# Optimization experiments

Hardware: AMD Instinct MI355X
Metric: run time of the kernel (lower is better)

The kernel has to match this reference:

```python
import jax, jax.numpy as jnp
import numpy as np


def _conv_s2(x, w):
    # NCHW input, OIHW weights, stride 2, VALID padding
    return jax.lax.conv_general_dilated(
        x, w, window_strides=(2, 2), padding='VALID',
        dimension_numbers=('NCHW', 'OIHW', 'NCHW'))


def setup_inputs() -> dict:
    key = jax.random.key(0)
    ks = jax.random.split(key, 9)
    B = 65536
    winit = lambda k, fan_in, shape: (jax.random.uniform(k, shape) - 0.5) * 2 * 2.4 / fan_in ** 0.5
    return {
        'x': jax.random.normal(ks[0], (B, 1, 16, 16), dtype=jnp.float32),
        'H1w': winit(ks[1], 5 * 5 * 1, (12, 1, 5, 5)),
        'H1b': jnp.zeros((12, 8, 8), dtype=jnp.float32),
        'H2w': winit(ks[2], 5 * 5 * 8, (12, 8, 5, 5)),
        'H2b': jnp.zeros((12, 4, 4), dtype=jnp.float32),
        'H3w': winit(ks[3], 4 * 4 * 12, (4 * 4 * 12, 30)),
        'H3b': jnp.zeros((30,), dtype=jnp.float32),
        'outw': winit(ks[4], 30, (30, 10)),
        'outb': -jnp.ones((10,), dtype=jnp.float32),
    }


def reference(x, H1w, H1b, H2w, H2b, H3w, H3b, outw, outb):
    NEG1_PAD = ((0, 0), (0, 0), (2, 2), (2, 2))
    # H1: pad 16->20 with -1, 5x5 conv stride 2 -> [B,12,8,8]
    x = jnp.pad(x, NEG1_PAD, constant_values=-1.0)
    x = jnp.tanh(_conv_s2(x, H1w) + H1b)
    # H2: pad 8->12 with -1, three group convs over 8-of-12 channels -> [B,12,4,4]
    x = jnp.pad(x, NEG1_PAD, constant_values=-1.0)
    s1 = _conv_s2(x[:, 0:8], H2w[0:4])
    s2 = _conv_s2(x[:, 4:12], H2w[4:8])
    s3 = _conv_s2(jnp.concatenate((x[:, 0:4], x[:, 8:12]), axis=1), H2w[8:12])
    x = jnp.tanh(jnp.concatenate((s1, s2, s3), axis=1) + H2b)
    # H3 + output MLP
    x = x.reshape(x.shape[0], -1)  # [B,192]
    x = jnp.tanh(x @ H3w + H3b)
    x = jnp.tanh(x @ outw + outb)
    return x
```

## Files before the change

### kernel.cpp

```cpp
#include <hip/hip_runtime.h>

typedef __attribute__((ext_vector_type(8))) short short8;
typedef __attribute__((ext_vector_type(4))) float f32x4;

#define SPB 4
#define NG  8
#define XP_S   400
#define A1_ROW 14
#define A1_CH  (12 * A1_ROW)
#define A1_S   (12 * A1_CH)
#define A2_S   200
#define A3_S   40

__device__ __forceinline__ float fast_tanh(float x) {
    float e = __builtin_amdgcn_exp2f(x * 2.8853900817779268f);
    return 1.0f - 2.0f * __builtin_amdgcn_rcpf(e + 1.0f);
}
__device__ __forceinline__ unsigned short f2bf(float f) {
    unsigned u = __builtin_bit_cast(unsigned, f);
    return (unsigned short)((u + 0x7FFF + ((u >> 16) & 1)) >> 16);
}


__global__ __launch_bounds__(256, 3) void lenet_mfma(
    const float* __restrict__ x,
    const float* __restrict__ w1, const float* __restrict__ b1,
    const float* __restrict__ w2, const float* __restrict__ b2,
    const float* __restrict__ w3, const float* __restrict__ b3,
    const float* __restrict__ ow, const float* __restrict__ ob,
    float* __restrict__ out)
{
    __shared__ __attribute__((aligned(16))) unsigned short wf3[6144];
    __shared__ __attribute__((aligned(16))) unsigned short xp[SPB * XP_S];
    __shared__ __attribute__((aligned(16))) unsigned short a1[SPB * A1_S];
    __shared__ __attribute__((aligned(16))) unsigned short a2[16 * A2_S];
    __shared__ __attribute__((aligned(16))) unsigned short a3[16 * A3_S];
    __shared__ float b1s[768], b2s[192], b3s[32], obs[16];

    const int t = threadIdx.x;
    const int lane = t & 63, wv = t >> 6;
    const int hi = lane >> 4, col = lane & 15;

    const float4* xg = (const float4*)(x + (size_t)blockIdx.x * NG * SPB * 256);
    float4 v0 = xg[t];

    int po1[4], po2[4];
    #pragma unroll
    for (int pp = 0; pp < 4; ++pp) {
        int P = 4 * hi + pp; if (P > 14) P = 14;
        int ky = P / 3, q = P - 3 * ky;
        po1[pp] = ky * 20 + 2 * q;
        po2[pp] = ky * A1_ROW + 2 * q;
    }

    short8 aw1;
    #pragma unroll
    for (int j = 0; j < 8; ++j) {
        int m = 8 * hi + j; float val = 0.f;
        if (m < 30 && col < 12) {
            int P = m >> 1, ky = P / 3, q = P - 3 * ky, c = 2 * q + (m & 1);
            if (c < 5) val = w1[col * 25 + ky * 5 + c];
        }
        aw1[j] = (short)f2bf(val);
    }
    short8 aw2[12];
    #pragma unroll
    for (int ic = 0; ic < 12; ++ic) {
        #pragma unroll
        for (int j = 0; j < 8; ++j) {
            int m = 8 * hi + j; float val = 0.f;
            if (m < 30 && col < 12) {
                int P = m >> 1, ky = P / 3, q = P - 3 * ky, c = 2 * q + (m & 1);
                if (c < 5) {
                    int oc = col, icw;
                    if (oc < 4)      icw = (ic < 8) ? ic : -1;
                    else if (oc < 8) icw = (ic >= 4) ? ic - 4 : -1;
                    else             icw = (ic < 4) ? ic : ((ic >= 8) ? ic - 4 : -1);
                    if (icw >= 0) val = w2[(oc * 8 + icw) * 25 + ky * 5 + c];
                }
            }
            aw2[ic][j] = (short)f2bf(val);
        }
    }
    short8 awo;
    #pragma unroll
    for (int j = 0; j < 8; ++j) {
        int k = 8 * hi + j;
        awo[j] = (short)f2bf((col < 10 && k < 30) ? ow[k * 10 + col] : 0.f);
    }

    for (int e = t; e < 768; e += 256) {
        int fi = e >> 6, le = e & 63;
        int rt = fi / 6, kt = fi - 6 * rt;
        int unit = rt * 16 + (le & 15);
        short8 v;
        #pragma unroll
        for (int j = 0; j < 8; ++j) {
            int k = kt * 32 + 8 * (le >> 4) + j;
            v[j] = (short)f2bf((unit < 30) ? w3[k * 30 + unit] : 0.f);
        }
        *((short8*)wf3 + e) = v;
    }

    {
        unsigned* xpw = (unsigned*)xp;
        for (int i = t; i < SPB * XP_S / 2; i += 256) xpw[i] = 0xBF80BF80u;
        unsigned* a1w = (unsigned*)a1;
        for (int i = t; i < SPB * A1_S / 2; i += 256) a1w[i] = 0xBF80BF80u;
        unsigned* a3w = (unsigned*)a3;
        for (int i = t; i < 16 * A3_S / 2; i += 256) a3w[i] = 0u;
        for (int i = t; i < 768; i += 256) b1s[i] = b1[i];
        if (t < 192) b2s[t] = b2[t];
        if (t < 32)  b3s[t] = (t < 30) ? b3[t] : 0.f;
        if (t < 16)  obs[t] = (t < 10) ? ob[t] : 0.f;
    }
    __syncthreads();

    const int q1 = 40 * (col >> 3) + 2 * (col & 7);
    const int q2 = 28 * (col >> 2) + 2 * (col & 3);
    const unsigned* xp32 = (const unsigned*)xp;
    const unsigned* a132 = (const unsigned*)a1;

    #pragma unroll 1
    for (int g = 0; g < NG; ++g) {
        {
            int r = (t >> 2) & 15, c4 = (t & 3) * 4;
            int base = wv * XP_S + (2 + r) * 20 + (2 + c4);
            unsigned* dst = (unsigned*)xp + (base >> 1);
            dst[0] = (unsigned)f2bf(v0.x) | ((unsigned)f2bf(v0.y) << 16);
            dst[1] = (unsigned)f2bf(v0.z) | ((unsigned)f2bf(v0.w) << 16);
        }
        if (g + 1 < NG) v0 = xg[(g + 1) * 256 + t];

        {
            int sbase = wv * XP_S + q1;
            #pragma unroll
            for (int pt = 0; pt < 4; ++pt) {
                int base = (sbase + pt * 80) >> 1;
                short8 b;
                #pragma unroll
                for (int pp = 0; pp < 4; ++pp) {
                    unsigned r = xp32[base + (po1[pp] >> 1)];
                    b[2 * pp]     = (short)(r & 0xffff);
                    b[2 * pp + 1] = (short)(r >> 16);
                }
                f32x4 acc = __builtin_amdgcn_mfma_f32_16x16x32_bf16(
                    aw1, b, (f32x4){0.f, 0.f, 0.f, 0.f}, 0, 0, 0);
                int p = pt * 16 + col;
                int oy = p >> 3, ox = p & 7;
                int wbase = wv * A1_S + (2 + oy) * A1_ROW + (2 + ox);
                #pragma unroll
                for (int jj = 0; jj < 4; ++jj) {
                    int oc = hi * 4 + jj;
                    if (oc < 12)
                        a1[wbase + oc * A1_CH] =
                            f2bf(fast_tanh(acc[jj] + b1s[oc * 64 + p]));
                }
            }
        }

        {
            int sbase = wv * A1_S + q2;
            f32x4 acc = {0.f, 0.f, 0.f, 0.f};
            #pragma unroll
            for (int ic = 0; ic < 12; ++ic) {
                int base = (sbase + ic * A1_CH) >> 1;
                short8 b;
                #pragma unroll
                for (int pp = 0; pp < 4; ++pp) {
                    unsigned r = a132[base + (po2[pp] >> 1)];
                    b[2 * pp]     = (short)(r & 0xffff);
                    b[2 * pp + 1] = (short)(r >> 16);
                }
                acc = __builtin_amdgcn_mfma_f32_16x16x32_bf16(aw2[ic], b, acc, 0, 0, 0);
            }
            int sg = (g & 3) * 4 + wv;
            #pragma unroll
            for (int jj = 0; jj < 4; ++jj) {
                int oc = hi * 4 + jj;
                if (oc < 12)
                    a2[sg * A2_S + oc * 16 + col] =
                        f2bf(fast_tanh(acc[jj] + b2s[oc * 16 + col]));
            }
        }

        if ((g & 3) == 3) {
            __syncthreads();
            if (wv < 2) {
                int rt = wv;
                f32x4 acc = {0.f, 0.f, 0.f, 0.f};
                #pragma unroll
                for (int kt = 0; kt < 6; ++kt) {
                    short8 a = *((const short8*)wf3 + (rt * 6 + kt) * 64 + lane);
                    short8 b = *(const short8*)&a2[col * A2_S + kt * 32 + 8 * hi];
                    acc = __builtin_amdgcn_mfma_f32_16x16x32_bf16(a, b, acc, 0, 0, 0);
                }
                #pragma unroll
                for (int jj = 0; jj < 4; ++jj) {
                    int unit = rt * 16 + hi * 4 + jj;
                    if (unit < 30)
                        a3[col * A3_S + unit] = f2bf(fast_tanh(acc[jj] + b3s[unit]));
                }
            }
            __syncthreads();
            if (wv == 0) {
                short8 b = *(const short8*)&a3[col * A3_S + 8 * hi];
                f32x4 acc = __builtin_amdgcn_mfma_f32_16x16x32_bf16(
                    awo, b, (f32x4){0.f, 0.f, 0.f, 0.f}, 0, 0, 0);
                size_t sw = (size_t)blockIdx.x * (NG * SPB) + (g >> 2) * 16 + col;
                #pragma unroll
                for (int jj = 0; jj < 4; ++jj) {
                    int row = hi * 4 + jj;
                    if (row < 10)
                        out[sw * 10 + row] = fast_tanh(acc[jj] + obs[row]);
                }
            }
            __syncthreads();
        }
    }
}

extern "C" void kernel_launch(void* const* d_in, const int* in_sizes, int n_in,
                              void* d_out, int out_size, void* d_ws, size_t ws_size,
                              hipStream_t stream) {
    const float* x  = (const float*)d_in[0];
    const float* w1 = (const float*)d_in[1];
    const float* b1 = (const float*)d_in[2];
    const float* w2 = (const float*)d_in[3];
    const float* b2 = (const float*)d_in[4];
    const float* w3 = (const float*)d_in[5];
    const float* b3 = (const float*)d_in[6];
    const float* ow = (const float*)d_in[7];
    const float* ob = (const float*)d_in[8];
    float* out = (float*)d_out;

    const int B = in_sizes[0] / 256;
    lenet_mfma<<<dim3(B / (SPB * NG)), dim3(256), 0, stream>>>(
        x, w1, b1, w2, b2, w3, b3, ow, ob, out);
}
```

Before: 111.7 us.

## Shrink LDS footprint, split H2 accumulation chains, and spread FC layers across all waves

Reduces the A1 row pitch from 14 to 12 and stores the H1 bias as bf16 to cut shared memory, and raises launch bounds from 3 to 4 blocks per CU. The H2 convolution now uses two independent MFMA accumulator chains to shorten dependency latency. The H3 and output layers run on all four waves, each handling its own four samples instead of waves 0-1 and wave 0 doing all sixteen. This trades some duplicated MFMA work (only 4 of 16 columns are useful) and bf16 bias rounding for less serialization and higher occupancy.

```diff
diff --git a/kernel.cpp b/kernel.cpp
--- a/kernel.cpp
+++ b/kernel.cpp
@@ -6,7 +6,7 @@
 #define SPB 4
 #define NG  8
 #define XP_S   400
-#define A1_ROW 14
+#define A1_ROW 12
 #define A1_CH  (12 * A1_ROW)
 #define A1_S   (12 * A1_CH)
 #define A2_S   200
@@ -20,9 +20,12 @@
     unsigned u = __builtin_bit_cast(unsigned, f);
     return (unsigned short)((u + 0x7FFF + ((u >> 16) & 1)) >> 16);
 }
-
-
-__global__ __launch_bounds__(256, 3) void lenet_mfma(
+__device__ __forceinline__ float bf2f(unsigned short h) {
+    return __builtin_bit_cast(float, (unsigned)h << 16);
+}
+
+
+__global__ __launch_bounds__(256, 4) void lenet_mfma(
     const float* __restrict__ x,
     const float* __restrict__ w1, const float* __restrict__ b1,
     const float* __restrict__ w2, const float* __restrict__ b2,
@@ -35,7 +38,8 @@
     __shared__ __attribute__((aligned(16))) unsigned short a1[SPB * A1_S];
     __shared__ __attribute__((aligned(16))) unsigned short a2[16 * A2_S];
     __shared__ __attribute__((aligned(16))) unsigned short a3[16 * A3_S];
-    __shared__ float b1s[768], b2s[192], b3s[32], obs[16];
+    __shared__ unsigned short b1s[768];
+    __shared__ float b2s[192], b3s[32], obs[16];
 
     const int t = threadIdx.x;
     const int lane = t & 63, wv = t >> 6;
@@ -109,7 +113,7 @@
         for (int i = t; i < SPB * A1_S / 2; i += 256) a1w[i] = 0xBF80BF80u;
         unsigned* a3w = (unsigned*)a3;
         for (int i = t; i < 16 * A3_S / 2; i += 256) a3w[i] = 0u;
-        for (int i = t; i < 768; i += 256) b1s[i] = b1[i];
+        for (int i = t; i < 768; i += 256) b1s[i] = f2bf(b1[i]);
         if (t < 192) b2s[t] = b2[t];
         if (t < 32)  b3s[t] = (t < 30) ? b3[t] : 0.f;
         if (t < 16)  obs[t] = (t < 10) ? ob[t] : 0.f;
@@ -117,14 +121,15 @@
     __syncthreads();
 
     const int q1 = 40 * (col >> 3) + 2 * (col & 7);
-    const int q2 = 28 * (col >> 2) + 2 * (col & 3);
+    const int q2 = 24 * (col >> 2) + 2 * (col & 3);
     const unsigned* xp32 = (const unsigned*)xp;
     const unsigned* a132 = (const unsigned*)a1;
+    const int colc = col & 3;
 
     #pragma unroll 1
     for (int g = 0; g < NG; ++g) {
         {
-            int r = (t >> 2) & 15, c4 = (t & 3) * 4;
+            int r = lane >> 2, c4 = (lane & 3) * 4;
             int base = wv * XP_S + (2 + r) * 20 + (2 + c4);
             unsigned* dst = (unsigned*)xp + (base >> 1);
             dst[0] = (unsigned)f2bf(v0.x) | ((unsigned)f2bf(v0.y) << 16);
@@ -154,64 +159,71 @@
                     int oc = hi * 4 + jj;
                     if (oc < 12)
                         a1[wbase + oc * A1_CH] =
-                            f2bf(fast_tanh(acc[jj] + b1s[oc * 64 + p]));
+                            f2bf(fast_tanh(acc[jj] + bf2f(b1s[oc * 64 + p])));
                 }
             }
         }
 
         {
             int sbase = wv * A1_S + q2;
-            f32x4 acc = {0.f, 0.f, 0.f, 0.f};
-            #pragma unroll
-            for (int ic = 0; ic < 12; ++ic) {
-                int base = (sbase + ic * A1_CH) >> 1;
-                short8 b;
+            f32x4 acc0 = {0.f, 0.f, 0.f, 0.f};
+            f32x4 acc1 = {0.f, 0.f, 0.f, 0.f};
+            #pragma unroll
+            for (int ic = 0; ic < 6; ++ic) {
+                int b0 = (sbase + ic * A1_CH) >> 1;
+                int b1i = (sbase + (ic + 6) * A1_CH) >> 1;
+                short8 p0, p1;
                 #pragma unroll
                 for (int pp = 0; pp < 4; ++pp) {
-                    unsigned r = a132[base + (po2[pp] >> 1)];
-                    b[2 * pp]     = (short)(r & 0xffff);
-                    b[2 * pp + 1] = (short)(r >> 16);
-                }
-                acc = __builtin_amdgcn_mfma_f32_16x16x32_bf16(aw2[ic], b, acc, 0, 0, 0);
-            }
-            int sg = (g & 3) * 4 + wv;
+                    unsigned r0 = a132[b0 + (po2[pp] >> 1)];
+                    unsigned r1 = a132[b1i + (po2[pp] >> 1)];
+                    p0[2 * pp]     = (short)(r0 & 0xffff);
+                    p0[2 * pp + 1] = (short)(r0 >> 16);
+                    p1[2 * pp]     = (short)(r1 & 0xffff);
+                    p1[2 * pp + 1] = (short)(r1 >> 16);
+                }
+                acc0 = __builtin_amdgcn_mfma_f32_16x16x32_bf16(aw2[ic], p0, acc0, 0, 0, 0);
+                acc1 = __builtin_amdgcn_mfma_f32_16x16x32_bf16(aw2[ic + 6], p1, acc1, 0, 0, 0);
+            }
+            int sg = wv * 4 + (g & 3);
             #pragma unroll
             for (int jj = 0; jj < 4; ++jj) {
                 int oc = hi * 4 + jj;
                 if (oc < 12)
                     a2[sg * A2_S + oc * 16 + col] =
-                        f2bf(fast_tanh(acc[jj] + b2s[oc * 16 + col]));
+                        f2bf(fast_tanh(acc0[jj] + acc1[jj] + b2s[oc * 16 + col]));
             }
         }
 
         if ((g & 3) == 3) {
             __syncthreads();
-            if (wv < 2) {
-                int rt = wv;
+            #pragma unroll
+            for (int rt = 0; rt < 2; ++rt) {
                 f32x4 acc = {0.f, 0.f, 0.f, 0.f};
                 #pragma unroll
                 for (int kt = 0; kt < 6; ++kt) {
                     short8 a = *((const short8*)wf3 + (rt * 6 + kt) * 64 + lane);
-                    short8 b = *(const short8*)&a2[col * A2_S + kt * 32 + 8 * hi];
+                    short8 b = *(const short8*)&a2[(wv * 4 + colc) * A2_S + kt * 32 + 8 * hi];
                     acc = __builtin_amdgcn_mfma_f32_16x16x32_bf16(a, b, acc, 0, 0, 0);
                 }
                 #pragma unroll
                 for (int jj = 0; jj < 4; ++jj) {
                     int unit = rt * 16 + hi * 4 + jj;
-                    if (unit < 30)
-                        a3[col * A3_S + unit] = f2bf(fast_tanh(acc[jj] + b3s[unit]));
+                    if (unit < 30 && col < 4)
+                        a3[(wv * 4 + col) * A3_S + unit] =
+                            f2bf(fast_tanh(acc[jj] + b3s[unit]));
                 }
             }
             __syncthreads();
-            if (wv == 0) {
-                short8 b = *(const short8*)&a3[col * A3_S + 8 * hi];
+            {
+                short8 b = *(const short8*)&a3[(wv * 4 + colc) * A3_S + 8 * hi];
                 f32x4 acc = __builtin_amdgcn_mfma_f32_16x16x32_bf16(
                     awo, b, (f32x4){0.f, 0.f, 0.f, 0.f}, 0, 0, 0);
-                size_t sw = (size_t)blockIdx.x * (NG * SPB) + (g >> 2) * 16 + col;
+                size_t sw = (size_t)blockIdx.x * (NG * SPB) + (g - 3) * 4 + 4 * col + wv;
                 #pragma unroll
                 for (int jj = 0; jj < 4; ++jj) {
                     int row = hi * 4 + jj;
-                    if (row < 10)
+                    if (row < 10 && col < 4)
                         out[sw * 10 + row] = fast_tanh(acc[jj] + obs[row]);
                 }
             }
```

Result: slower. 270.7 us (+142.3%).
